# Kernel optimization log

Measured on AMD Instinct MI355X. Metric: run time of the kernel, lower is better.

The kernel has to match this reference:

```python
import jax, jax.numpy as jnp
import numpy as np

D_MODEL = 1024
DIM_K = 128
DIM_V = 128

def setup_inputs() -> dict:
    key = jax.random.key(0)
    ks = jax.random.split(key, 8)
    B, T = 4, 2048
    s = 1.0 / np.sqrt(D_MODEL)
    return {
        "X_Q": jax.random.normal(ks[0], (B, T, D_MODEL), jnp.float32),
        "X_KV": jax.random.normal(ks[1], (B, T, D_MODEL), jnp.float32),
        "Wq": jax.random.normal(ks[2], (D_MODEL, DIM_K), jnp.float32) * s,
        "bq": jnp.zeros((DIM_K,), jnp.float32),
        "Wk": jax.random.normal(ks[3], (D_MODEL, DIM_K), jnp.float32) * s,
        "bk": jnp.zeros((DIM_K,), jnp.float32),
        "Wv": jax.random.normal(ks[4], (D_MODEL, DIM_V), jnp.float32) * s,
        "bv": jnp.zeros((DIM_V,), jnp.float32),
    }

def reference(X_Q, X_KV, Wq, bq, Wk, bk, Wv, bv):
    T = X_Q.shape[1]
    Q = X_Q @ Wq + bq                      # [B, T, dk]
    K = X_KV @ Wk + bk                     # [B, T, dk]
    V = X_KV @ Wv + bv                     # [B, T, dv]
    scale = 1.0 / jnp.sqrt(jnp.float32(DIM_K))
    scores = jnp.einsum('bqd,bkd->bqk', Q, K) * scale  # [B, T, T]
    causal = jnp.tril(jnp.ones((T, T), bool))
    scores = jnp.where(causal, scores, -jnp.inf)
    attn = jax.nn.softmax(scores, axis=-1)
    return jnp.einsum('bqk,bkd->bqd', attn, V)         # [B, T, dv]
```

## Files before the change

kernel.cpp:

```cpp
#include <hip/hip_runtime.h>
#include <hip/hip_bf16.h>
#include <math.h>

#define BT 8192
#define TT 2048
#define DM 1024
#define DK 128
#define NBLK 65

typedef __bf16 bf16x8 __attribute__((ext_vector_type(8)));
typedef float  f32x4  __attribute__((ext_vector_type(4)));
typedef unsigned short ushort4v __attribute__((ext_vector_type(4)));
typedef unsigned short ushort8v __attribute__((ext_vector_type(8)));

static __device__ __forceinline__ unsigned short f2bf(float x) {
    union { float f; unsigned u; } v; v.f = x;
    unsigned r = v.u + 0x7fffu + ((v.u >> 16) & 1u);
    return (unsigned short)(r >> 16);
}
static __device__ __forceinline__ float bf2f(unsigned short u) {
    union { unsigned u; float f; } v; v.u = (unsigned)u << 16;
    return v.f;
}

__host__ __device__ constexpr int slc_of(int q) { return (q == 0) ? 1 : ((q + 1) >> 1); }
__host__ __device__ constexpr int pfx_of(int q) { return (q == 0) ? 0 : 1 + (q * q - (q & 1)) / 4; }

#define QSCALE 0.1275312772629451f

__global__ __launch_bounds__(256) void wt_prep(
    const float* __restrict__ Wq, const float* __restrict__ Wk,
    const float* __restrict__ Wv, unsigned short* __restrict__ Wt)
{
    const int z = blockIdx.y;
    const float* __restrict__ W = (z == 0) ? Wq : (z == 1 ? Wk : Wv);
    const int k0 = blockIdx.x * 64;

    __shared__ __align__(16) __bf16 T[128][72];
    const int t = threadIdx.x;

#pragma unroll
    for (int jj = 0; jj < 8; ++jj) {
        int c  = jj * 256 + t;
        int k  = c >> 5;
        int n4 = (c & 31) * 4;
        float4 f = *reinterpret_cast<const float4*>(&W[(size_t)(k0 + k) * DK + n4]);
        T[n4 + 0][k] = (__bf16)f.x;
        T[n4 + 1][k] = (__bf16)f.y;
        T[n4 + 2][k] = (__bf16)f.z;
        T[n4 + 3][k] = (__bf16)f.w;
    }
    __syncthreads();

    const int n  = t >> 1;
    const int cb = (t & 1) * 32;
#pragma unroll
    for (int jj = 0; jj < 4; ++jj) {
        *reinterpret_cast<ushort8v*>(&Wt[((size_t)z * DK + n) * DM + k0 + cb + jj * 8]) =
            *reinterpret_cast<const ushort8v*>(&T[n][cb + jj * 8]);
    }
}

__global__ __launch_bounds__(256) void proj_mfma(
    const float* __restrict__ XQ, const float* __restrict__ XKV,
    const unsigned short* __restrict__ Wt,
    const float* __restrict__ bq, const float* __restrict__ bk,
    const float* __restrict__ bv,
    unsigned short* __restrict__ Qb, unsigned short* __restrict__ Kb,
    unsigned short* __restrict__ Vt)
{
    const int z = blockIdx.y;
    const float* __restrict__ X    = (z == 0) ? XQ : XKV;
    const float* __restrict__ bias = (z == 0) ? bq : (z == 1 ? bk : bv);
    const unsigned short* __restrict__ Wz = Wt + (size_t)z * DK * DM;

    __shared__ __align__(16) __bf16 Xl[64][72];
    __shared__ __align__(16) __bf16 Wl[128][72];

    const int t    = threadIdx.x;
    const int lane = t & 63;
    const int wv   = t >> 6;
    const int i16  = lane & 15;
    const int g    = lane >> 4;
    const int m0   = blockIdx.x * 64;

    f32x4 acc[8];
#pragma unroll
    for (int nt = 0; nt < 8; ++nt) acc[nt] = (f32x4){0.f, 0.f, 0.f, 0.f};

    for (int k0 = 0; k0 < DM; k0 += 64) {
        {
            int r  = t >> 2;
            int cb = (t & 3) * 16;
            const float4* src = reinterpret_cast<const float4*>(
                &X[(size_t)(m0 + r) * DM + k0 + cb]);
            float4 f0 = src[0], f1 = src[1], f2 = src[2], f3 = src[3];
            __bf16 tmp[16];
            tmp[0]  = (__bf16)f0.x; tmp[1]  = (__bf16)f0.y;
            tmp[2]  = (__bf16)f0.z; tmp[3]  = (__bf16)f0.w;
            tmp[4]  = (__bf16)f1.x; tmp[5]  = (__bf16)f1.y;
            tmp[6]  = (__bf16)f1.z; tmp[7]  = (__bf16)f1.w;
            tmp[8]  = (__bf16)f2.x; tmp[9]  = (__bf16)f2.y;
            tmp[10] = (__bf16)f2.z; tmp[11] = (__bf16)f2.w;
            tmp[12] = (__bf16)f3.x; tmp[13] = (__bf16)f3.y;
            tmp[14] = (__bf16)f3.z; tmp[15] = (__bf16)f3.w;
            *reinterpret_cast<bf16x8*>(&Xl[r][cb])     = *reinterpret_cast<bf16x8*>(&tmp[0]);
            *reinterpret_cast<bf16x8*>(&Xl[r][cb + 8]) = *reinterpret_cast<bf16x8*>(&tmp[8]);
        }
        {
            int n  = t >> 1;
            int cb = (t & 1) * 32;
            const ushort8v* src = reinterpret_cast<const ushort8v*>(
                &Wz[(size_t)n * DM + k0 + cb]);
            ushort8v w0 = src[0], w1 = src[1], w2 = src[2], w3 = src[3];
            *reinterpret_cast<ushort8v*>(&Wl[n][cb + 0])  = w0;
            *reinterpret_cast<ushort8v*>(&Wl[n][cb + 8])  = w1;
            *reinterpret_cast<ushort8v*>(&Wl[n][cb + 16]) = w2;
            *reinterpret_cast<ushort8v*>(&Wl[n][cb + 24]) = w3;
        }
        __syncthreads();

#pragma unroll
        for (int c = 0; c < 2; ++c) {
            bf16x8 xf = *reinterpret_cast<const bf16x8*>(&Xl[wv * 16 + i16][c * 32 + g * 8]);
#pragma unroll
            for (int nt = 0; nt < 8; ++nt) {
                bf16x8 wf = *reinterpret_cast<const bf16x8*>(&Wl[nt * 16 + i16][c * 32 + g * 8]);
                acc[nt] = __builtin_amdgcn_mfma_f32_16x16x32_bf16(xf, wf, acc[nt], 0, 0, 0);
            }
        }
        __syncthreads();
    }

    if (z == 0) {
#pragma unroll
        for (int nt = 0; nt < 8; ++nt) {
            int n = nt * 16 + i16;
            float bb = bias[n];
#pragma unroll
            for (int r = 0; r < 4; ++r) {
                int mrow = m0 + wv * 16 + g * 4 + r;
                Qb[(size_t)mrow * DK + n] = f2bf((acc[nt][r] + bb) * QSCALE);
            }
        }
    } else if (z == 1) {
#pragma unroll
        for (int nt = 0; nt < 8; ++nt) {
            int n = nt * 16 + i16;
            float bb = bias[n];
#pragma unroll
            for (int r = 0; r < 4; ++r) {
                int mrow = m0 + wv * 16 + g * 4 + r;
                Kb[(size_t)mrow * DK + n] = f2bf(acc[nt][r] + bb);
            }
        }
    } else {
        const int b  = m0 / TT;
        const int t0 = (m0 % TT) + wv * 16 + g * 4;
#pragma unroll
        for (int nt = 0; nt < 8; ++nt) {
            int d = nt * 16 + i16;
            float bb = bias[d];
            ushort4v r;
#pragma unroll
            for (int e = 0; e < 4; ++e) r[e] = f2bf(acc[nt][e] + bb);
            *reinterpret_cast<ushort4v*>(&Vt[((size_t)b * DK + d) * TT + t0]) = r;
        }
    }
}

__global__ __launch_bounds__(512, 2) void attn_kernel(
    const unsigned short* __restrict__ Qb, const unsigned short* __restrict__ Kb,
    const unsigned short* __restrict__ Vt,
    unsigned short* __restrict__ pO, float* __restrict__ pMS)
{
    __shared__ __align__(16) unsigned short lds_[2][16384];

    const int t    = threadIdx.x;
    const int lane = t & 63;
    const int w    = t >> 6;
    const int qi   = lane & 15;
    const int g    = lane >> 4;

    const int bi    = blockIdx.x;
    const int batch = bi / NBLK;
    const int rr    = bi - batch * NBLK;
    int qbl = 0;
#pragma unroll
    for (int i = 1; i < 16; ++i) if (rr >= pfx_of(i)) qbl = i;
    const int slice = rr - (qbl == 0 ? 0 : 1 + (qbl * qbl - (qbl & 1)) / 4);
    const int S     = (qbl == 0) ? 1 : ((qbl + 1) >> 1);
    const int nch   = 2 * qbl + 2;
    const int q0    = qbl * 128;

    const unsigned short* __restrict__ Kbb = Kb + (size_t)batch * TT * DK;
    const unsigned short* __restrict__ Vtb = Vt + (size_t)batch * DK * TT;

    const int qrow  = q0 + w * 16 + qi;
    const int qminw = q0 + w * 16;
    const int qmaxw = q0 + w * 16 + 15;

    bf16x8 qf[4];
#pragma unroll
    for (int c = 0; c < 4; ++c)
        qf[c] = *reinterpret_cast<const bf16x8*>(
            &Qb[((size_t)batch * TT + qrow) * DK + c * 32 + g * 8]);

    f32x4 accO[8];
#pragma unroll
    for (int dt = 0; dt < 8; ++dt) accO[dt] = (f32x4){0.f, 0.f, 0.f, 0.f};
    float m = -1e30f, s = 0.f;

    ushort8v sreg[4];
    const int kslot0 = (w & 3) * 256;

#define STAGE_ISSUE(c_)                                                         \
    {                                                                           \
        const int k0s = (c_) * 64;                                              \
        if (w < 4) {                                                            \
            _Pragma("unroll")                                                   \
            for (int i = 0; i < 4; ++i) {                                       \
                int slot = kslot0 + i * 64 + lane;                              \
                int row  = slot >> 4;                                           \
                int colg = (slot & 15) ^ (row & 15);                            \
                sreg[i] = *reinterpret_cast<const ushort8v*>(                   \
                    &Kbb[(size_t)(k0s + row) * DK + colg * 8]);                 \
            }                                                                   \
        } else {                                                                \
            _Pragma("unroll")                                                   \
            for (int i = 0; i < 4; ++i) {                                       \
                int slot = kslot0 + i * 64 + lane;                              \
                int row  = slot >> 3;                                           \
                int colg = (slot & 7) ^ (row & 7);                              \
                sreg[i] = *reinterpret_cast<const ushort8v*>(                   \
                    &Vtb[(size_t)row * TT + k0s + colg * 8]);                   \
            }                                                                   \
        }                                                                       \
    }

#define STAGE_WRITE(buf_)                                                       \
    {                                                                           \
        const int base = (w < 4) ? 0 : 8192;                                    \
        _Pragma("unroll")                                                       \
        for (int i = 0; i < 4; ++i) {                                           \
            int slot = kslot0 + i * 64 + lane;                                  \
            *reinterpret_cast<ushort8v*>(&lds_[buf_][base + slot * 8]) = sreg[i]; \
        }                                                                       \
    }

    STAGE_ISSUE(slice);
    STAGE_WRITE(0);
    __syncthreads();

    int buf = 0;
    for (int c = slice; c < nch; c += S) {
        const int cn = c + S;
        if (cn < nch) STAGE_ISSUE(cn);

        const int k0 = c * 64;
        if (k0 <= qmaxw) {
            f32x4 accS[4];
#pragma unroll
            for (int ks = 0; ks < 4; ++ks) accS[ks] = (f32x4){0.f, 0.f, 0.f, 0.f};
#pragma unroll
            for (int cc = 0; cc < 4; ++cc) {
#pragma unroll
                for (int ks = 0; ks < 4; ++ks) {
                    bf16x8 kf = *reinterpret_cast<const bf16x8*>(
                        &lds_[buf][(ks * 16 + qi) * 128 + ((cc * 4 + g) ^ qi) * 8]);
                    accS[ks] = __builtin_amdgcn_mfma_f32_16x16x32_bf16(kf, qf[cc], accS[ks], 0, 0, 0);
                }
            }

            float xmax = -1e30f;
            if (k0 + 63 > qminw) {
#pragma unroll
                for (int ks = 0; ks < 4; ++ks)
#pragma unroll
                    for (int r = 0; r < 4; ++r) {
                        int k = k0 + ks * 16 + g * 4 + r;
                        float v0 = (k <= qrow) ? accS[ks][r] : -1e30f;
                        accS[ks][r] = v0;
                        xmax = fmaxf(xmax, v0);
                    }
            } else {
#pragma unroll
                for (int ks = 0; ks < 4; ++ks)
#pragma unroll
                    for (int r = 0; r < 4; ++r) xmax = fmaxf(xmax, accS[ks][r]);
            }

            if (__any(xmax > m + 8.f)) {
                xmax = fmaxf(xmax, __shfl_xor(xmax, 16));
                xmax = fmaxf(xmax, __shfl_xor(xmax, 32));
                float mn   = fmaxf(m, xmax);
                float corr = __builtin_amdgcn_exp2f(m - mn);
                s *= corr;
#pragma unroll
                for (int dt = 0; dt < 8; ++dt)
#pragma unroll
                    for (int e = 0; e < 4; ++e) accO[dt][e] *= corr;
                m = mn;
            }

            unsigned pk[8];
#pragma unroll
            for (int ks = 0; ks < 4; ++ks)
#pragma unroll
                for (int h = 0; h < 2; ++h) {
                    float plo = __builtin_amdgcn_exp2f(accS[ks][h * 2]     - m);
                    float phi = __builtin_amdgcn_exp2f(accS[ks][h * 2 + 1] - m);
                    s += plo + phi;
                    pk[ks * 2 + h] = (unsigned)f2bf(plo) | ((unsigned)f2bf(phi) << 16);
                }

            const int srcl0 = qi + 32 * (g & 1);
            bf16x8 pf[2];
#pragma unroll
            for (int c2 = 0; c2 < 2; ++c2) {
                union { unsigned u[4]; bf16x8 v; } pu;
#pragma unroll
                for (int w4 = 0; w4 < 4; ++w4) {
                    int srcl = srcl0 + 16 * (w4 >> 1);
                    int a = __shfl((int)pk[c2 * 4 + (w4 & 1)],     srcl);
                    int b = __shfl((int)pk[c2 * 4 + 2 + (w4 & 1)], srcl);
                    pu.u[w4] = (g & 2) ? (unsigned)b : (unsigned)a;
                }
                pf[c2] = pu.v;
            }

#pragma unroll
            for (int dt = 0; dt < 8; ++dt) {
#pragma unroll
                for (int c2 = 0; c2 < 2; ++c2) {
                    bf16x8 vf = *reinterpret_cast<const bf16x8*>(
                        &lds_[buf][8192 + (dt * 16 + qi) * 64 + ((c2 * 4 + g) ^ (qi & 7)) * 8]);
                    accO[dt] = __builtin_amdgcn_mfma_f32_16x16x32_bf16(vf, pf[c2], accO[dt], 0, 0, 0);
                }
            }
        }

        if (cn < nch) STAGE_WRITE(buf ^ 1);
        __syncthreads();
        buf ^= 1;
    }

    float srow = s + __shfl_xor(s, 16);
    srow += __shfl_xor(srow, 32);

    const size_t prow = (size_t)bi * 128 + w * 16 + qi;
    if (g == 0) {
        pMS[prow * 2]     = m;
        pMS[prow * 2 + 1] = srow;
    }
#pragma unroll
    for (int dt = 0; dt < 8; ++dt) {
        ushort4v r;
#pragma unroll
        for (int e = 0; e < 4; ++e) r[e] = f2bf(accO[dt][e]);
        *reinterpret_cast<ushort4v*>(&pO[prow * DK + dt * 16 + g * 4]) = r;
    }
#undef STAGE_ISSUE
#undef STAGE_WRITE
}

__global__ __launch_bounds__(256) void attn_combine(
    const unsigned short* __restrict__ pO, const float* __restrict__ pMS,
    float* __restrict__ O)
{
    const int t  = threadIdx.x;
    const int r  = blockIdx.x * 8 + (t >> 5);
    const int dq = (t & 31) * 4;

    const int batch = r >> 11;
    const int qbl   = (r >> 7) & 15;
    const int lr    = r & 127;
    const int S     = (qbl == 0) ? 1 : ((qbl + 1) >> 1);
    const int base  = batch * NBLK + (qbl == 0 ? 0 : 1 + (qbl * qbl - (qbl & 1)) / 4);

    float mstar = -1e30f;
    for (int ss = 0; ss < S; ++ss)
        mstar = fmaxf(mstar, pMS[((size_t)(base + ss) * 128 + lr) * 2]);

    float den = 0.f;
    float num[4] = {0.f, 0.f, 0.f, 0.f};
    for (int ss = 0; ss < S; ++ss) {
        const size_t pr = (size_t)(base + ss) * 128 + lr;
        float ms = pMS[pr * 2];
        float sv = pMS[pr * 2 + 1];
        float wgt = __builtin_amdgcn_exp2f(ms - mstar);
        den += wgt * sv;
        ushort4v ov = *reinterpret_cast<const ushort4v*>(&pO[pr * DK + dq]);
#pragma unroll
        for (int e = 0; e < 4; ++e) num[e] += wgt * bf2f(ov[e]);
    }

    const float inv = 1.f / den;
    float4 out;
    out.x = num[0] * inv; out.y = num[1] * inv;
    out.z = num[2] * inv; out.w = num[3] * inv;
    *reinterpret_cast<float4*>(&O[(size_t)r * DK + dq]) = out;
}

extern "C" void kernel_launch(void* const* d_in, const int* in_sizes, int n_in,
                              void* d_out, int out_size, void* d_ws, size_t ws_size,
                              hipStream_t stream) {
    const float* XQ  = (const float*)d_in[0];
    const float* XKV = (const float*)d_in[1];
    const float* Wq  = (const float*)d_in[2];
    const float* bq  = (const float*)d_in[3];
    const float* Wk  = (const float*)d_in[4];
    const float* bk  = (const float*)d_in[5];
    const float* Wv  = (const float*)d_in[6];
    const float* bv  = (const float*)d_in[7];

    unsigned short* Qb = (unsigned short*)d_ws;
    unsigned short* Kb = Qb + (size_t)BT * DK;
    unsigned short* Vt = Kb + (size_t)BT * DK;
    unsigned short* Wt = Vt + (size_t)BT * DK;
    float*          pMS = (float*)(Wt + (size_t)3 * DK * DM);
    unsigned short* pO  = (unsigned short*)(pMS + (size_t)4 * NBLK * 128 * 2);

    wt_prep<<<dim3(16, 3), 256, 0, stream>>>(Wq, Wk, Wv, Wt);

    proj_mfma<<<dim3(BT / 64, 3), 256, 0, stream>>>(
        XQ, XKV, Wt, bq, bk, bv, Qb, Kb, Vt);

    attn_kernel<<<dim3(4 * NBLK), 512, 0, stream>>>(Qb, Kb, Vt, pO, pMS);

    attn_combine<<<dim3(BT / 8), 256, 0, stream>>>(pO, pMS, (float*)d_out);
}
```

Baseline: 65.86 us.

## Double-buffer weight tiles and load X directly into registers in projection

The projection GEMM now double-buffers the weight tile in LDS and prefetches the next K-slice of both W and X into registers while MFMAs run on the current slice. X rows are read straight from global memory into each wave's registers, because each wave only uses its own 16 rows; this removes the X LDS staging buffer and its writes. Launch bounds now request 4 blocks per CU. The intent is to hide global load latency behind compute. The cost is higher register pressure, which may spill under the tighter occupancy bound.

```diff
diff --git a/kernel.cpp b/kernel.cpp
--- a/kernel.cpp
+++ b/kernel.cpp
@@ -61,7 +61,7 @@
     }
 }
 
-__global__ __launch_bounds__(256) void proj_mfma(
+__global__ __launch_bounds__(256, 4) void proj_mfma(
     const float* __restrict__ XQ, const float* __restrict__ XKV,
     const unsigned short* __restrict__ Wt,
     const float* __restrict__ bq, const float* __restrict__ bk,
@@ -74,8 +74,7 @@
     const float* __restrict__ bias = (z == 0) ? bq : (z == 1 ? bk : bv);
     const unsigned short* __restrict__ Wz = Wt + (size_t)z * DK * DM;
 
-    __shared__ __align__(16) __bf16 Xl[64][72];
-    __shared__ __align__(16) __bf16 Wl[128][72];
+    __shared__ __align__(16) __bf16 Wl[2][128][72];
 
     const int t    = threadIdx.x;
     const int lane = t & 63;
@@ -84,53 +83,80 @@
     const int g    = lane >> 4;
     const int m0   = blockIdx.x * 64;
 
+    const float* __restrict__ Xrow =
+        X + (size_t)(m0 + wv * 16 + i16) * DM + g * 8;
+    const unsigned short* __restrict__ Wrow =
+        Wz + (size_t)(t >> 1) * DM + (t & 1) * 32;
+
     f32x4 acc[8];
 #pragma unroll
     for (int nt = 0; nt < 8; ++nt) acc[nt] = (f32x4){0.f, 0.f, 0.f, 0.f};
 
-    for (int k0 = 0; k0 < DM; k0 += 64) {
-        {
-            int r  = t >> 2;
-            int cb = (t & 3) * 16;
-            const float4* src = reinterpret_cast<const float4*>(
-                &X[(size_t)(m0 + r) * DM + k0 + cb]);
-            float4 f0 = src[0], f1 = src[1], f2 = src[2], f3 = src[3];
-            __bf16 tmp[16];
-            tmp[0]  = (__bf16)f0.x; tmp[1]  = (__bf16)f0.y;
-            tmp[2]  = (__bf16)f0.z; tmp[3]  = (__bf16)f0.w;
-            tmp[4]  = (__bf16)f1.x; tmp[5]  = (__bf16)f1.y;
-            tmp[6]  = (__bf16)f1.z; tmp[7]  = (__bf16)f1.w;
-            tmp[8]  = (__bf16)f2.x; tmp[9]  = (__bf16)f2.y;
-            tmp[10] = (__bf16)f2.z; tmp[11] = (__bf16)f2.w;
-            tmp[12] = (__bf16)f3.x; tmp[13] = (__bf16)f3.y;
-            tmp[14] = (__bf16)f3.z; tmp[15] = (__bf16)f3.w;
-            *reinterpret_cast<bf16x8*>(&Xl[r][cb])     = *reinterpret_cast<bf16x8*>(&tmp[0]);
-            *reinterpret_cast<bf16x8*>(&Xl[r][cb + 8]) = *reinterpret_cast<bf16x8*>(&tmp[8]);
-        }
-        {
-            int n  = t >> 1;
-            int cb = (t & 1) * 32;
-            const ushort8v* src = reinterpret_cast<const ushort8v*>(
-                &Wz[(size_t)n * DM + k0 + cb]);
-            ushort8v w0 = src[0], w1 = src[1], w2 = src[2], w3 = src[3];
-            *reinterpret_cast<ushort8v*>(&Wl[n][cb + 0])  = w0;
-            *reinterpret_cast<ushort8v*>(&Wl[n][cb + 8])  = w1;
-            *reinterpret_cast<ushort8v*>(&Wl[n][cb + 16]) = w2;
-            *reinterpret_cast<ushort8v*>(&Wl[n][cb + 24]) = w3;
-        }
+    float4   xa[4], xb[4];
+    ushort8v wr_[4];
+
+#define LOADX(xr_, k0_)                                                        \
+    {                                                                          \
+        _Pragma("unroll")                                                      \
+        for (int c = 0; c < 2; ++c)                                            \
+            _Pragma("unroll")                                                  \
+            for (int h = 0; h < 2; ++h)                                        \
+                xr_[c * 2 + h] = *reinterpret_cast<const float4*>(             \
+                    &Xrow[(k0_) + c * 32 + h * 4]);                            \
+    }
+#define LOADW(k0_)                                                             \
+    {                                                                          \
+        _Pragma("unroll")                                                      \
+        for (int i = 0; i < 4; ++i)                                            \
+            wr_[i] = *reinterpret_cast<const ushort8v*>(&Wrow[(k0_) + i * 8]); \
+    }
+#define WRITEW(buf_)                                                           \
+    {                                                                          \
+        _Pragma("unroll")                                                      \
+        for (int i = 0; i < 4; ++i)                                            \
+            *reinterpret_cast<ushort8v*>(                                      \
+                &Wl[buf_][t >> 1][(t & 1) * 32 + i * 8]) = wr_[i];             \
+    }
+#define COMPUTE(xr_, buf_)                                                     \
+    {                                                                          \
+        _Pragma("unroll")                                                      \
+        for (int c = 0; c < 2; ++c) {                                          \
+            union { __bf16 b[8]; bf16x8 v; } u;                                \
+            u.b[0] = (__bf16)xr_[c * 2].x;  u.b[1] = (__bf16)xr_[c * 2].y;     \
+            u.b[2] = (__bf16)xr_[c * 2].z;  u.b[3] = (__bf16)xr_[c * 2].w;     \
+            u.b[4] = (__bf16)xr_[c * 2 + 1].x; u.b[5] = (__bf16)xr_[c * 2 + 1].y; \
+            u.b[6] = (__bf16)xr_[c * 2 + 1].z; u.b[7] = (__bf16)xr_[c * 2 + 1].w; \
+            _Pragma("unroll")                                                  \
+            for (int nt = 0; nt < 8; ++nt) {                                   \
+                bf16x8 wf = *reinterpret_cast<const bf16x8*>(                  \
+                    &Wl[buf_][nt * 16 + i16][c * 32 + g * 8]);                 \
+                acc[nt] = __builtin_amdgcn_mfma_f32_16x16x32_bf16(u.v, wf, acc[nt], 0, 0, 0); \
+            }                                                                  \
+        }                                                                      \
+    }
+
+    LOADX(xa, 0);
+    LOADW(0);
+    WRITEW(0);
+    __syncthreads();
+    LOADW(64);
+    LOADX(xb, 64);
+
+#pragma unroll
+    for (int t2 = 0; t2 < 16; t2 += 2) {
+        COMPUTE(xa, 0);
+        WRITEW(1);
         __syncthreads();
-
-#pragma unroll
-        for (int c = 0; c < 2; ++c) {
-            bf16x8 xf = *reinterpret_cast<const bf16x8*>(&Xl[wv * 16 + i16][c * 32 + g * 8]);
-#pragma unroll
-            for (int nt = 0; nt < 8; ++nt) {
-                bf16x8 wf = *reinterpret_cast<const bf16x8*>(&Wl[nt * 16 + i16][c * 32 + g * 8]);
-                acc[nt] = __builtin_amdgcn_mfma_f32_16x16x32_bf16(xf, wf, acc[nt], 0, 0, 0);
-            }
-        }
+        if (t2 + 2 < 16) { LOADW((t2 + 2) * 64); LOADX(xa, (t2 + 2) * 64); }
+        COMPUTE(xb, 1);
+        if (t2 + 3 < 16) WRITEW(0);
         __syncthreads();
-    }
+        if (t2 + 3 < 16) { LOADW((t2 + 3) * 64); LOADX(xb, (t2 + 3) * 64); }
+    }
+#undef LOADX
+#undef LOADW
+#undef WRITEW
+#undef COMPUTE
 
     if (z == 0) {
 #pragma unroll
```

After: 61.66 us. 1.07x faster.

## Load projection MFMA operands directly from global memory, dropping LDS staging

Applied to the files above, without the earlier changes.

The projection kernel no longer stages X and W tiles through shared memory with barriers. Each lane now loads its own MFMA fragments straight from global memory, converting X to bf16 in registers, and the K loop is fully unrolled. This removes LDS traffic and the two __syncthreads per iteration, so loads can overlap compute. In exchange, W fragments are fetched redundantly by all four waves and the accesses are less coalesced, which relies on L1/L2 hits and adds register pressure.

```diff
diff --git a/kernel.cpp b/kernel.cpp
--- a/kernel.cpp
+++ b/kernel.cpp
@@ -74,9 +74,6 @@
     const float* __restrict__ bias = (z == 0) ? bq : (z == 1 ? bk : bv);
     const unsigned short* __restrict__ Wz = Wt + (size_t)z * DK * DM;
 
-    __shared__ __align__(16) __bf16 Xl[64][72];
-    __shared__ __align__(16) __bf16 Wl[128][72];
-
     const int t    = threadIdx.x;
     const int lane = t & 63;
     const int wv   = t >> 6;
@@ -84,52 +81,45 @@
     const int g    = lane >> 4;
     const int m0   = blockIdx.x * 64;
 
+    const float* __restrict__ Xrow =
+        X + (size_t)(m0 + wv * 16 + i16) * DM + g * 8;
+    const unsigned short* __restrict__ Wrow =
+        Wz + (size_t)i16 * DM + g * 8;
+
     f32x4 acc[8];
 #pragma unroll
     for (int nt = 0; nt < 8; ++nt) acc[nt] = (f32x4){0.f, 0.f, 0.f, 0.f};
 
+#pragma unroll
     for (int k0 = 0; k0 < DM; k0 += 64) {
-        {
-            int r  = t >> 2;
-            int cb = (t & 3) * 16;
-            const float4* src = reinterpret_cast<const float4*>(
-                &X[(size_t)(m0 + r) * DM + k0 + cb]);
-            float4 f0 = src[0], f1 = src[1], f2 = src[2], f3 = src[3];
-            __bf16 tmp[16];
-            tmp[0]  = (__bf16)f0.x; tmp[1]  = (__bf16)f0.y;
-            tmp[2]  = (__bf16)f0.z; tmp[3]  = (__bf16)f0.w;
-            tmp[4]  = (__bf16)f1.x; tmp[5]  = (__bf16)f1.y;
-            tmp[6]  = (__bf16)f1.z; tmp[7]  = (__bf16)f1.w;
-            tmp[8]  = (__bf16)f2.x; tmp[9]  = (__bf16)f2.y;
-            tmp[10] = (__bf16)f2.z; tmp[11] = (__bf16)f2.w;
-            tmp[12] = (__bf16)f3.x; tmp[13] = (__bf16)f3.y;
-            tmp[14] = (__bf16)f3.z; tmp[15] = (__bf16)f3.w;
-            *reinterpret_cast<bf16x8*>(&Xl[r][cb])     = *reinterpret_cast<bf16x8*>(&tmp[0]);
-            *reinterpret_cast<bf16x8*>(&Xl[r][cb + 8]) = *reinterpret_cast<bf16x8*>(&tmp[8]);
+        float4 xr[4];
+#pragma unroll
+        for (int c = 0; c < 2; ++c)
+#pragma unroll
+            for (int h = 0; h < 2; ++h)
+                xr[c * 2 + h] = *reinterpret_cast<const float4*>(
+                    &Xrow[k0 + c * 32 + h * 4]);
+
+        bf16x8 wf[16];
+#pragma unroll
+        for (int c = 0; c < 2; ++c)
+#pragma unroll
+            for (int nt = 0; nt < 8; ++nt)
+                wf[c * 8 + nt] = *reinterpret_cast<const bf16x8*>(
+                    &Wrow[(size_t)nt * 16 * DM + k0 + c * 32]);
+
+#pragma unroll
+        for (int c = 0; c < 2; ++c) {
+            union { __bf16 b[8]; bf16x8 v; } u;
+            u.b[0] = (__bf16)xr[c * 2].x;     u.b[1] = (__bf16)xr[c * 2].y;
+            u.b[2] = (__bf16)xr[c * 2].z;     u.b[3] = (__bf16)xr[c * 2].w;
+            u.b[4] = (__bf16)xr[c * 2 + 1].x; u.b[5] = (__bf16)xr[c * 2 + 1].y;
+            u.b[6] = (__bf16)xr[c * 2 + 1].z; u.b[7] = (__bf16)xr[c * 2 + 1].w;
+#pragma unroll
+            for (int nt = 0; nt < 8; ++nt)
+                acc[nt] = __builtin_amdgcn_mfma_f32_16x16x32_bf16(
+                    u.v, wf[c * 8 + nt], acc[nt], 0, 0, 0);
         }
-        {
-            int n  = t >> 1;
-            int cb = (t & 1) * 32;
-            const ushort8v* src = reinterpret_cast<const ushort8v*>(
-                &Wz[(size_t)n * DM + k0 + cb]);
-            ushort8v w0 = src[0], w1 = src[1], w2 = src[2], w3 = src[3];
-            *reinterpret_cast<ushort8v*>(&Wl[n][cb + 0])  = w0;
-            *reinterpret_cast<ushort8v*>(&Wl[n][cb + 8])  = w1;
-            *reinterpret_cast<ushort8v*>(&Wl[n][cb + 16]) = w2;
-            *reinterpret_cast<ushort8v*>(&Wl[n][cb + 24]) = w3;
-        }
-        __syncthreads();
-
-#pragma unroll
-        for (int c = 0; c < 2; ++c) {
-            bf16x8 xf = *reinterpret_cast<const bf16x8*>(&Xl[wv * 16 + i16][c * 32 + g * 8]);
-#pragma unroll
-            for (int nt = 0; nt < 8; ++nt) {
-                bf16x8 wf = *reinterpret_cast<const bf16x8*>(&Wl[nt * 16 + i16][c * 32 + g * 8]);
-                acc[nt] = __builtin_amdgcn_mfma_f32_16x16x32_bf16(xf, wf, acc[nt], 0, 0, 0);
-            }
-        }
-        __syncthreads();
     }
 
     if (z == 0) {
```

Result: slower. 109.3 us (+65.9%).
